# Kernel optimization log

Measured on AMD Instinct MI355X. Metric: run time of the kernel, lower is better.

Reference implementation:

```python
import jax, jax.numpy as jnp
import numpy as np

# Graph sizes: users -> items ('ui') and users -> tags ('ut'), plus reverse etypes.
N_U, N_I, N_T, D = 100000, 50000, 20000, 128
E_UI, E_UT = 500000, 300000


def setup_inputs() -> dict:
    key = jax.random.key(0)
    k = jax.random.split(key, 7)
    return {
        "h_u": jax.random.normal(k[0], (N_U, D), jnp.float32),
        "h_i": jax.random.normal(k[1], (N_I, D), jnp.float32),
        "h_t": jax.random.normal(k[2], (N_T, D), jnp.float32),
        "ui_src": jax.random.randint(k[3], (E_UI,), 0, N_U, jnp.int32),
        "ui_dst": jax.random.randint(k[4], (E_UI,), 0, N_I, jnp.int32),
        "ut_src": jax.random.randint(k[5], (E_UT,), 0, N_U, jnp.int32),
        "ut_dst": jax.random.randint(k[6], (E_UT,), 0, N_T, jnp.int32),
    }


def _seg_sum(x, idx, n):
    return jax.ops.segment_sum(x, idx, num_segments=n)


def _deg(idx, n):
    # in-degree, clamped to min 1 (as torch .clamp(min=1))
    return jnp.clip(_seg_sum(jnp.ones(idx.shape, jnp.float32), idx, n), 1.0, None)


def reference(h_u, h_i, h_t, ui_src, ui_dst, ut_src, ut_dst):
    NORM_2 = -1.0  # default norm_2 arg
    # forward pass: copy_u('h') + sum per etype, then 1/in_degree normalization on dst
    rst_i = _seg_sum(h_u[ui_src], ui_dst, N_I) / _deg(ui_dst, N_I)[:, None]  # [N_I, D]
    rst_t = _seg_sum(h_u[ut_src], ut_dst, N_T) / _deg(ut_dst, N_T)[:, None]  # [N_T, D]
    # backward pass: multi_update_all over reverse etypes, 'sum' cross-etype reducer
    bsrc = _seg_sum(rst_i[ui_dst], ui_src, N_U) + _seg_sum(rst_t[ut_dst], ut_src, N_U)
    # in_degrees_b: per-etype clamped degrees summed across reverse etypes
    deg_b = _deg(ui_src, N_U) + _deg(ut_src, N_U)
    bsrc = bsrc * (deg_b ** NORM_2)[:, None]
    # rst is the LAST etype's normalized dst result ('ut' -> tags)
    return bsrc, rst_t
```

## Files before the change

### kernel.cpp

```cpp
#include <hip/hip_runtime.h>

#define NU 100000
#define NI 50000
#define NT 20000
#define DD 128
#define EUI 500000
#define EUT 300000

#define B_I   0
#define B_T   (NI)
#define B_UUI (NI + NT)
#define B_UUT (NI + NT + NU)
#define NSCAN (NI + NT + NU + NU)
#define TOTAL_E (2 * (EUI + EUT))

#define BPB   512
#define NB    ((NSCAN + BPB - 1) / BPB)
#define CH    8192
#define NBLK  ((TOTAL_E + CH - 1) / CH)
#define NHIST (NB * NBLK)

__device__ __forceinline__ unsigned bfpack(float a, float b) {
    unsigned ua = __float_as_uint(a), ub = __float_as_uint(b);
    ua = (ua + 0x7FFFu + ((ua >> 16) & 1u)) >> 16;
    ub = (ub + 0x7FFFu + ((ub >> 16) & 1u)) >> 16;
    return ua | (ub << 16);
}
__device__ __forceinline__ void bacc(unsigned p, float& a, float& b) {
    a += __uint_as_float(p << 16);
    b += __uint_as_float(p & 0xFFFF0000u);
}

__device__ __forceinline__ void entry_of(int e,
        const int* __restrict__ ui_src, const int* __restrict__ ui_dst,
        const int* __restrict__ ut_src, const int* __restrict__ ut_dst,
        int& bucket, int& val) {
    if (e < EUI)              { bucket = B_I   + ui_dst[e];              val = ui_src[e]; }
    else if (e < 2 * EUI)     { int j = e - EUI;       bucket = B_UUI + ui_src[j]; val = ui_dst[j]; }
    else if (e < 2 * EUI + EUT){ int j = e - 2 * EUI;   bucket = B_T   + ut_dst[j]; val = ut_src[j]; }
    else                      { int j = e - 2 * EUI - EUT; bucket = B_UUT + ut_src[j]; val = ut_dst[j]; }
}

__global__ void k_hist(const int* __restrict__ ui_src, const int* __restrict__ ui_dst,
                       const int* __restrict__ ut_src, const int* __restrict__ ut_dst,
                       int* __restrict__ hist) {
    __shared__ int h[NB];
    int b = blockIdx.x, t = threadIdx.x;
    for (int i = t; i < NB; i += 256) h[i] = 0;
    __syncthreads();
    int e0 = b * CH;
    int e1 = min(e0 + CH, TOTAL_E);
    for (int e = e0 + t; e < e1; e += 256) {
        int bucket, val;
        entry_of(e, ui_src, ui_dst, ut_src, ut_dst, bucket, val);
        (void)val;
        atomicAdd(&h[bucket >> 9], 1);
    }
    __syncthreads();
    for (int i = t; i < NB; i += 256) hist[i * NBLK + b] = h[i];
}

__global__ void k_scanA(int* __restrict__ data, int* __restrict__ bsums, int n) {
    __shared__ int lds[256];
    int b = blockIdx.x, t = threadIdx.x;
    int base = b * 1024 + t * 4;
    int v0 = (base + 0 < n) ? data[base + 0] : 0;
    int v1 = (base + 1 < n) ? data[base + 1] : 0;
    int v2 = (base + 2 < n) ? data[base + 2] : 0;
    int v3 = (base + 3 < n) ? data[base + 3] : 0;
    int i0 = v0, i1 = i0 + v1, i2 = i1 + v2, i3 = i2 + v3;
    lds[t] = i3;
    __syncthreads();
    for (int o = 1; o < 256; o <<= 1) {
        int x = (t >= o) ? lds[t - o] : 0;
        __syncthreads();
        lds[t] += x;
        __syncthreads();
    }
    int ex = lds[t] - i3;
    if (base + 0 < n) data[base + 0] = ex + i0;
    if (base + 1 < n) data[base + 1] = ex + i1;
    if (base + 2 < n) data[base + 2] = ex + i2;
    if (base + 3 < n) data[base + 3] = ex + i3;
    if (t == 255) bsums[b] = lds[255];
}

__global__ void k_scanB(int* __restrict__ bsums, int nsb) {
    __shared__ int lds[512];
    int t = threadIdx.x;
    int a = (t < nsb) ? bsums[t] : 0;
    int b2 = (t + 256 < nsb) ? bsums[t + 256] : 0;
    lds[t] = a;
    lds[t + 256] = b2;
    __syncthreads();
    for (int o = 1; o < 512; o <<= 1) {
        int x0 = (t >= o) ? lds[t - o] : 0;
        int x1 = (t + 256 >= o) ? lds[t + 256 - o] : 0;
        __syncthreads();
        lds[t] += x0;
        lds[t + 256] += x1;
        __syncthreads();
    }
    if (t < nsb) bsums[t] = lds[t] - a;
    if (t + 256 < nsb) bsums[t + 256] = lds[t + 256] - b2;
}

__global__ void k_scanC(int* __restrict__ data, const int* __restrict__ bsums, int n) {
    int b = blockIdx.x;
    int add = bsums[b];
    int base = b * 1024 + threadIdx.x * 4;
    if (base + 0 < n) data[base + 0] += add;
    if (base + 1 < n) data[base + 1] += add;
    if (base + 2 < n) data[base + 2] += add;
    if (base + 3 < n) data[base + 3] += add;
}

__global__ void k_scatterbin(const int* __restrict__ ui_src, const int* __restrict__ ui_dst,
                             const int* __restrict__ ut_src, const int* __restrict__ ut_dst,
                             const int* __restrict__ hist, unsigned* __restrict__ binned) {
    __shared__ int loff[NB];
    int b = blockIdx.x, t = threadIdx.x;
    for (int i = t; i < NB; i += 256) loff[i] = hist[i * NBLK + b];
    __syncthreads();
    int e0 = b * CH;
    int e1 = min(e0 + CH, TOTAL_E);
    for (int e = e0 + t; e < e1; e += 256) {
        int bucket, val;
        entry_of(e, ui_src, ui_dst, ut_src, ut_dst, bucket, val);
        int bin = bucket >> 9;
        int pos = atomicAdd(&loff[bin], -1) - 1;
        binned[pos] = ((unsigned)(bucket & (BPB - 1)) << 17) | (unsigned)val;
    }
}

__global__ void k_bincount(const unsigned* __restrict__ binned,
                           const int* __restrict__ hist, int* __restrict__ off) {
    __shared__ int cnt[BPB];
    int b = blockIdx.x, t = threadIdx.x;
    cnt[t] = 0; cnt[t + 256] = 0;
    __syncthreads();
    int s = (b == 0) ? 0 : hist[b * NBLK - 1];
    int e = hist[(b + 1) * NBLK - 1];
    for (int i = s + t; i < e; i += 256) atomicAdd(&cnt[binned[i] >> 17], 1);
    __syncthreads();
    int base = b * BPB;
    if (base + t < NSCAN) off[base + t] = cnt[t];
    if (base + t + 256 < NSCAN) off[base + t + 256] = cnt[t + 256];
}

__global__ void k_finescatter(const unsigned* __restrict__ binned,
                              const int* __restrict__ hist,
                              int* __restrict__ off, int* __restrict__ edges) {
    __shared__ int loff[BPB];
    int b = blockIdx.x, t = threadIdx.x;
    int base = b * BPB;
    if (base + t < NSCAN) loff[t] = off[base + t];
    if (base + t + 256 < NSCAN) loff[t + 256] = off[base + t + 256];
    __syncthreads();
    int s = (b == 0) ? 0 : hist[b * NBLK - 1];
    int e = hist[(b + 1) * NBLK - 1];
    for (int i = s + t; i < e; i += 256) {
        unsigned v = binned[i];
        int local = v >> 17;
        int pos = atomicAdd(&loff[local], -1) - 1;
        edges[pos] = (int)(v & 0x1FFFFu);
    }
    __syncthreads();
    if (base + t < NSCAN) off[base + t] = loff[t];
    if (base + t + 256 < NSCAN) off[base + t + 256] = loff[t + 256];
}

__global__ void k_cvt(const float4* __restrict__ in, uint4* __restrict__ out) {
    int t = blockIdx.x * blockDim.x + threadIdx.x;
    if (t >= NU * DD / 8) return;
    float4 a = in[t * 2 + 0];
    float4 b = in[t * 2 + 1];
    uint4 o;
    o.x = bfpack(a.x, a.y); o.y = bfpack(a.z, a.w);
    o.z = bfpack(b.x, b.y); o.w = bfpack(b.z, b.w);
    out[t] = o;
}


__global__ void g_fwd(const uint4* __restrict__ feat,
                      const int* __restrict__ off, const int* __restrict__ edges,
                      uint4* __restrict__ rsti_b, uint4* __restrict__ rstt_b,
                      float4* __restrict__ outf) {
    int tid = blockIdx.x * blockDim.x + threadIdx.x;
    int r = tid >> 4;
    int c = tid & 15;
    if (r >= NI + NT) return;
    int start = off[r];
    int end = off[r + 1];
    float a0=0.f,a1=0.f,a2=0.f,a3=0.f,a4=0.f,a5=0.f,a6=0.f,a7=0.f;
    for (int base = start; base < end; base += 16) {
        int n = min(16, end - base);
        int eidx = (c < n) ? edges[base + c] : 0;
        #pragma unroll 4
        for (int k = 0; k < n; ++k) {
            int s = __shfl(eidx, k, 16);
            uint4 p = feat[(size_t)s * 16 + c];
            bacc(p.x, a0, a1); bacc(p.y, a2, a3);
            bacc(p.z, a4, a5); bacc(p.w, a6, a7);
        }
    }
    float inv = 1.0f / fmaxf((float)(end - start), 1.0f);
    a0*=inv; a1*=inv; a2*=inv; a3*=inv; a4*=inv; a5*=inv; a6*=inv; a7*=inv;
    uint4 ob;
    ob.x = bfpack(a0,a1); ob.y = bfpack(a2,a3);
    ob.z = bfpack(a4,a5); ob.w = bfpack(a6,a7);
    if (r < NI) {
        rsti_b[(size_t)r * 16 + c] = ob;
    } else {
        int rt = r - NI;
        rstt_b[(size_t)rt * 16 + c] = ob;
        float4 f0; f0.x=a0; f0.y=a1; f0.z=a2; f0.w=a3;
        float4 f1; f1.x=a4; f1.y=a5; f1.z=a6; f1.w=a7;
        outf[(size_t)rt * 32 + c*2 + 0] = f0;
        outf[(size_t)rt * 32 + c*2 + 1] = f1;
    }
}

__global__ void g_bwd(const uint4* __restrict__ rst_i, const uint4* __restrict__ rst_t,
                      const int* __restrict__ off, const int* __restrict__ edges,
                      float4* __restrict__ bsrc) {
    int tid = blockIdx.x * blockDim.x + threadIdx.x;
    int r = tid >> 4;
    int c = tid & 15;
    if (r >= NU) return;
    int s1 = off[B_UUI + r], e1 = off[B_UUI + r + 1];
    int g2 = B_UUT + r;
    int s2 = off[g2], e2 = (g2 + 1 < NSCAN) ? off[g2 + 1] : TOTAL_E;
    float a0=0.f,a1=0.f,a2=0.f,a3=0.f,a4=0.f,a5=0.f,a6=0.f,a7=0.f;
    for (int base = s1; base < e1; base += 16) {
        int n = min(16, e1 - base);
        int eidx = (c < n) ? edges[base + c] : 0;
        #pragma unroll 4
        for (int k = 0; k < n; ++k) {
            int d = __shfl(eidx, k, 16);
            uint4 p = rst_i[(size_t)d * 16 + c];
            bacc(p.x, a0, a1); bacc(p.y, a2, a3);
            bacc(p.z, a4, a5); bacc(p.w, a6, a7);
        }
    }
    for (int base = s2; base < e2; base += 16) {
        int n = min(16, e2 - base);
        int eidx = (c < n) ? edges[base + c] : 0;
        #pragma unroll 4
        for (int k = 0; k < n; ++k) {
            int d = __shfl(eidx, k, 16);
            uint4 p = rst_t[(size_t)d * 16 + c];
            bacc(p.x, a0, a1); bacc(p.y, a2, a3);
            bacc(p.z, a4, a5); bacc(p.w, a6, a7);
        }
    }
    float inv = 1.0f / (fmaxf((float)(e1 - s1), 1.0f) + fmaxf((float)(e2 - s2), 1.0f));
    float4 f0; f0.x=a0*inv; f0.y=a1*inv; f0.z=a2*inv; f0.w=a3*inv;
    float4 f1; f1.x=a4*inv; f1.y=a5*inv; f1.z=a6*inv; f1.w=a7*inv;
    bsrc[(size_t)r * 32 + c*2 + 0] = f0;
    bsrc[(size_t)r * 32 + c*2 + 1] = f1;
}

__global__ void k_count_old(const int4* __restrict__ ui_src, const int4* __restrict__ ui_dst,
                            const int4* __restrict__ ut_src, const int4* __restrict__ ut_dst,
                            int* __restrict__ off) {
    int i = blockIdx.x * blockDim.x + threadIdx.x;
    if (i < EUI / 4) {
        int4 s = ui_src[i], d = ui_dst[i];
        atomicAdd(&off[B_I + d.x], 1); atomicAdd(&off[B_I + d.y], 1);
        atomicAdd(&off[B_I + d.z], 1); atomicAdd(&off[B_I + d.w], 1);
        atomicAdd(&off[B_UUI + s.x], 1); atomicAdd(&off[B_UUI + s.y], 1);
        atomicAdd(&off[B_UUI + s.z], 1); atomicAdd(&off[B_UUI + s.w], 1);
    } else if (i < EUI / 4 + EUT / 4) {
        int j = i - EUI / 4;
        int4 s = ut_src[j], d = ut_dst[j];
        atomicAdd(&off[B_T + d.x], 1); atomicAdd(&off[B_T + d.y], 1);
        atomicAdd(&off[B_T + d.z], 1); atomicAdd(&off[B_T + d.w], 1);
        atomicAdd(&off[B_UUT + s.x], 1); atomicAdd(&off[B_UUT + s.y], 1);
        atomicAdd(&off[B_UUT + s.z], 1); atomicAdd(&off[B_UUT + s.w], 1);
    }
}

__global__ void k_fill_old(const int2* __restrict__ ui_src, const int2* __restrict__ ui_dst,
                           const int2* __restrict__ ut_src, const int2* __restrict__ ut_dst,
                           int* __restrict__ off, int* __restrict__ edges) {
    int i = blockIdx.x * blockDim.x + threadIdx.x;
    if (i < EUI / 2) {
        int2 s = ui_src[i], d = ui_dst[i];
        edges[atomicAdd(&off[B_I + d.x], -1) - 1] = s.x;
        edges[atomicAdd(&off[B_UUI + s.x], -1) - 1] = d.x;
        edges[atomicAdd(&off[B_I + d.y], -1) - 1] = s.y;
        edges[atomicAdd(&off[B_UUI + s.y], -1) - 1] = d.y;
    } else if (i < EUI / 2 + EUT / 2) {
        int j = i - EUI / 2;
        int2 s = ut_src[j], d = ut_dst[j];
        edges[atomicAdd(&off[B_T + d.x], -1) - 1] = s.x;
        edges[atomicAdd(&off[B_UUT + s.x], -1) - 1] = d.x;
        edges[atomicAdd(&off[B_T + d.y], -1) - 1] = s.y;
        edges[atomicAdd(&off[B_UUT + s.y], -1) - 1] = d.y;
    }
}

__global__ void k_gather_fwd_f(const float4* __restrict__ feat,
                               const int* __restrict__ off, const int* __restrict__ edges,
                               uint2* __restrict__ outb, float4* __restrict__ outf,
                               int base, int nrows) {
    int tid = blockIdx.x * blockDim.x + threadIdx.x;
    int r = tid >> 5;
    int c = tid & 31;
    if (r >= nrows) return;
    int g = base + r;
    int start = off[g];
    int end = (g + 1 < NSCAN) ? off[g + 1] : TOTAL_E;
    float a0 = 0.f, a1 = 0.f, a2 = 0.f, a3 = 0.f;
    for (int e = start; e < end; ++e) {
        float4 v = feat[(size_t)edges[e] * 32 + c];
        a0 += v.x; a1 += v.y; a2 += v.z; a3 += v.w;
    }
    float inv = 1.0f / fmaxf((float)(end - start), 1.0f);
    a0 *= inv; a1 *= inv; a2 *= inv; a3 *= inv;
    uint2 ob; ob.x = bfpack(a0, a1); ob.y = bfpack(a2, a3);
    outb[(size_t)r * 32 + c] = ob;
    if (outf) {
        float4 of; of.x = a0; of.y = a1; of.z = a2; of.w = a3;
        outf[(size_t)r * 32 + c] = of;
    }
}

__global__ void k_gather_bwd_b(const uint2* __restrict__ rst_i,
                               const uint2* __restrict__ rst_t,
                               const int* __restrict__ off, const int* __restrict__ edges,
                               float4* __restrict__ bsrc) {
    int tid = blockIdx.x * blockDim.x + threadIdx.x;
    int r = tid >> 5;
    int c = tid & 31;
    if (r >= NU) return;
    int g1 = B_UUI + r;
    int s1 = off[g1], e1 = off[g1 + 1];
    int g2 = B_UUT + r;
    int s2 = off[g2], e2 = (g2 + 1 < NSCAN) ? off[g2 + 1] : TOTAL_E;
    float a0 = 0.f, a1 = 0.f, a2 = 0.f, a3 = 0.f;
    for (int e = s1; e < e1; ++e) {
        uint2 p = rst_i[(size_t)edges[e] * 32 + c];
        bacc(p.x, a0, a1); bacc(p.y, a2, a3);
    }
    for (int e = s2; e < e2; ++e) {
        uint2 p = rst_t[(size_t)edges[e] * 32 + c];
        bacc(p.x, a0, a1); bacc(p.y, a2, a3);
    }
    float inv = 1.0f / (fmaxf((float)(e1 - s1), 1.0f) + fmaxf((float)(e2 - s2), 1.0f));
    float4 o;
    o.x = a0 * inv; o.y = a1 * inv; o.z = a2 * inv; o.w = a3 * inv;
    bsrc[(size_t)r * 32 + c] = o;
}

__global__ void f_count(const int* __restrict__ ui_src, const int* __restrict__ ui_dst,
                        const int* __restrict__ ut_src, const int* __restrict__ ut_dst,
                        float* __restrict__ cnt_uui, float* __restrict__ cnt_i,
                        float* __restrict__ cnt_uut, float* __restrict__ cnt_t) {
    int i = blockIdx.x * blockDim.x + threadIdx.x;
    if (i < EUI) {
        unsafeAtomicAdd(&cnt_uui[ui_src[i]], 1.0f);
        unsafeAtomicAdd(&cnt_i[ui_dst[i]], 1.0f);
    } else if (i < EUI + EUT) {
        int j = i - EUI;
        unsafeAtomicAdd(&cnt_uut[ut_src[j]], 1.0f);
        unsafeAtomicAdd(&cnt_t[ut_dst[j]], 1.0f);
    }
}
__global__ void f_scatter_fwd(const float4* __restrict__ feat, const int* __restrict__ src,
                              const int* __restrict__ dst, float* __restrict__ out_sum, int nedge) {
    int tid = blockIdx.x * blockDim.x + threadIdx.x;
    int e = tid >> 5, c = tid & 31;
    if (e >= nedge) return;
    float4 v = feat[(size_t)src[e] * 32 + c];
    float* o = out_sum + (size_t)dst[e] * DD + c * 4;
    unsafeAtomicAdd(o + 0, v.x); unsafeAtomicAdd(o + 1, v.y);
    unsafeAtomicAdd(o + 2, v.z); unsafeAtomicAdd(o + 3, v.w);
}
__global__ void f_scatter_bwd(const float4* __restrict__ rst_sum, const float* __restrict__ cnt,
                              const int* __restrict__ src, const int* __restrict__ dst,
                              float* __restrict__ bsrc, int nedge) {
    int tid = blockIdx.x * blockDim.x + threadIdx.x;
    int e = tid >> 5, c = tid & 31;
    if (e >= nedge) return;
    float inv = 1.0f / fmaxf(cnt[dst[e]], 1.0f);
    float4 v = rst_sum[(size_t)dst[e] * 32 + c];
    float* o = bsrc + (size_t)src[e] * DD + c * 4;
    unsafeAtomicAdd(o + 0, v.x * inv); unsafeAtomicAdd(o + 1, v.y * inv);
    unsafeAtomicAdd(o + 2, v.z * inv); unsafeAtomicAdd(o + 3, v.w * inv);
}
__global__ void f_norm(float4* __restrict__ rst, const float* __restrict__ cnt, int nrows) {
    int tid = blockIdx.x * blockDim.x + threadIdx.x;
    int r = tid >> 5, c = tid & 31;
    if (r >= nrows) return;
    float inv = 1.0f / fmaxf(cnt[r], 1.0f);
    float4 v = rst[(size_t)r * 32 + c];
    v.x *= inv; v.y *= inv; v.z *= inv; v.w *= inv;
    rst[(size_t)r * 32 + c] = v;
}
__global__ void f_final(float4* __restrict__ bsrc, const float* __restrict__ cnt_a,
                        const float* __restrict__ cnt_b, int nrows) {
    int tid = blockIdx.x * blockDim.x + threadIdx.x;
    int r = tid >> 5, c = tid & 31;
    if (r >= nrows) return;
    float inv = 1.0f / (fmaxf(cnt_a[r], 1.0f) + fmaxf(cnt_b[r], 1.0f));
    float4 v = bsrc[(size_t)r * 32 + c];
    v.x *= inv; v.y *= inv; v.z *= inv; v.w *= inv;
    bsrc[(size_t)r * 32 + c] = v;
}


extern "C" void kernel_launch(void* const* d_in, const int* in_sizes, int n_in,
                              void* d_out, int out_size, void* d_ws, size_t ws_size,
                              hipStream_t stream) {
    const float* h_u  = (const float*)d_in[0];
    const int* ui_src = (const int*)d_in[3];
    const int* ui_dst = (const int*)d_in[4];
    const int* ut_src = (const int*)d_in[5];
    const int* ut_dst = (const int*)d_in[6];

    float* bsrc  = (float*)d_out;
    float* rst_t = (float*)d_out + (size_t)NU * DD;

    const int B = 256;

    const size_t INT_WORDS = (size_t)NSCAN + 512 + TOTAL_E;
    const size_t BASE_B    = INT_WORDS * 4;
    const size_t HUB_B     = (size_t)NU * DD * 2;
    const size_t RIB_B     = (size_t)NI * DD * 2;
    const size_t RTB_B     = (size_t)NT * DD * 2;
    const size_t NEED_FULL = BASE_B + HUB_B + RIB_B + RTB_B;
    const size_t NEED_HALF = BASE_B + RIB_B + RTB_B;

    if (ws_size >= NEED_FULL) {
        int* off      = (int*)d_ws;
        int* bsums    = off + NSCAN;
        int* edges    = bsums + 512;
        uint4* hu_b   = (uint4*)((char*)d_ws + BASE_B);
        uint4* rsti_b = (uint4*)((char*)d_ws + BASE_B + HUB_B);
        uint4* rstt_b = (uint4*)((char*)d_ws + BASE_B + HUB_B + RIB_B);
        unsigned* binned = (unsigned*)rsti_b;
        int* hist        = (int*)rstt_b;

        k_cvt<<<(NU * DD / 8 + B - 1) / B, B, 0, stream>>>(
            (const float4*)h_u, hu_b);

        k_hist<<<NBLK, B, 0, stream>>>(ui_src, ui_dst, ut_src, ut_dst, hist);

        {
            int nblk = (NHIST + 1023) / 1024;
            k_scanA<<<nblk, B, 0, stream>>>(hist, bsums, NHIST);
            k_scanB<<<1, B, 0, stream>>>(bsums, nblk);
            k_scanC<<<nblk, B, 0, stream>>>(hist, bsums, NHIST);
        }

        k_scatterbin<<<NBLK, B, 0, stream>>>(ui_src, ui_dst, ut_src, ut_dst, hist, binned);

        k_bincount<<<NB, B, 0, stream>>>(binned, hist, off);

        {
            int nblk = (NSCAN + 1023) / 1024;
            k_scanA<<<nblk, B, 0, stream>>>(off, bsums, NSCAN);
            k_scanB<<<1, B, 0, stream>>>(bsums, nblk);
            k_scanC<<<nblk, B, 0, stream>>>(off, bsums, NSCAN);
        }

        k_finescatter<<<NB, B, 0, stream>>>(binned, hist, off, edges);

        g_fwd<<<((long)(NI + NT) * 16 + B - 1) / B, B, 0, stream>>>(
            hu_b, off, edges, rsti_b, rstt_b, (float4*)rst_t);
        g_bwd<<<((long)NU * 16 + B - 1) / B, B, 0, stream>>>(
            rsti_b, rstt_b, off, edges, (float4*)bsrc);
    } else if (ws_size >= NEED_HALF) {
        int* off   = (int*)d_ws;
        int* bsums = off + NSCAN;
        int* edges = bsums + 512;
        uint2* rsti_b = (uint2*)((char*)d_ws + BASE_B);
        uint2* rstt_b = (uint2*)((char*)d_ws + BASE_B + RIB_B);

        hipMemsetAsync(off, 0, (NSCAN + 512) * sizeof(int), stream);

        int nq = EUI / 4 + EUT / 4;
        k_count_old<<<(nq + B - 1) / B, B, 0, stream>>>(
            (const int4*)ui_src, (const int4*)ui_dst,
            (const int4*)ut_src, (const int4*)ut_dst, off);
        {
            int nblk = (NSCAN + 1023) / 1024;
            k_scanA<<<nblk, B, 0, stream>>>(off, bsums, NSCAN);
            k_scanB<<<1, B, 0, stream>>>(bsums, nblk);
            k_scanC<<<nblk, B, 0, stream>>>(off, bsums, NSCAN);
        }
        int nh = EUI / 2 + EUT / 2;
        k_fill_old<<<(nh + B - 1) / B, B, 0, stream>>>(
            (const int2*)ui_src, (const int2*)ui_dst,
            (const int2*)ut_src, (const int2*)ut_dst, off, edges);

        k_gather_fwd_f<<<((long)NI * 32 + B - 1) / B, B, 0, stream>>>(
            (const float4*)h_u, off, edges, rsti_b, (float4*)nullptr, B_I, NI);
        k_gather_fwd_f<<<((long)NT * 32 + B - 1) / B, B, 0, stream>>>(
            (const float4*)h_u, off, edges, rstt_b, (float4*)rst_t, B_T, NT);
        k_gather_bwd_b<<<((long)NU * 32 + B - 1) / B, B, 0, stream>>>(
            rsti_b, rstt_b, off, edges, (float4*)bsrc);
    } else {
        float* ws        = (float*)d_ws;
        float* rst_i_sum = ws;
        float* cnt_i     = rst_i_sum + (size_t)NI * DD;
        float* cnt_t     = cnt_i + NI;
        float* cnt_uui   = cnt_t + NT;
        float* cnt_uut   = cnt_uui + NU;
        size_t ws_floats = (size_t)NI * DD + NI + NT + NU + NU;

        hipMemsetAsync(d_ws, 0, ws_floats * sizeof(float), stream);
        hipMemsetAsync(d_out, 0, (size_t)out_size * sizeof(float), stream);

        int n = EUI + EUT;
        f_count<<<(n + B - 1) / B, B, 0, stream>>>(ui_src, ui_dst, ut_src, ut_dst,
                                                   cnt_uui, cnt_i, cnt_uut, cnt_t);
        f_scatter_fwd<<<((long)EUI * 32 + B - 1) / B, B, 0, stream>>>(
            (const float4*)h_u, ui_src, ui_dst, rst_i_sum, EUI);
        f_scatter_fwd<<<((long)EUT * 32 + B - 1) / B, B, 0, stream>>>(
            (const float4*)h_u, ut_src, ut_dst, rst_t, EUT);
        f_scatter_bwd<<<((long)EUI * 32 + B - 1) / B, B, 0, stream>>>(
            (const float4*)rst_i_sum, cnt_i, ui_src, ui_dst, bsrc, EUI);
        f_scatter_bwd<<<((long)EUT * 32 + B - 1) / B, B, 0, stream>>>(
            (const float4*)rst_t, cnt_t, ut_src, ut_dst, bsrc, EUT);
        f_norm<<<((long)NT * 32 + B - 1) / B, B, 0, stream>>>((float4*)rst_t, cnt_t, NT);
        f_final<<<((long)NU * 32 + B - 1) / B, B, 0, stream>>>((float4*)bsrc, cnt_uui, cnt_uut, NU);
    }
}
```

Measured before the change: 182.7 us.

## Simplify CSR build to global-bin atomics and unroll gather loops by eight

```diff
diff --git a/kernel.cpp b/kernel.cpp
--- a/kernel.cpp
+++ b/kernel.cpp
@@ -18,7 +18,7 @@
 #define NB    ((NSCAN + BPB - 1) / BPB)
 #define CH    8192
 #define NBLK  ((TOTAL_E + CH - 1) / CH)
-#define NHIST (NB * NBLK)
+#define NT3   176
 
 __device__ __forceinline__ unsigned bfpack(float a, float b) {
     unsigned ua = __float_as_uint(a), ub = __float_as_uint(b);
@@ -31,143 +31,124 @@
     b += __uint_as_float(p & 0xFFFF0000u);
 }
 
+__device__ __forceinline__ int bucket_of(int e,
+        const int* __restrict__ ui_src, const int* __restrict__ ui_dst,
+        const int* __restrict__ ut_src, const int* __restrict__ ut_dst) {
+    if (e < EUI)               return B_I   + ui_dst[e];
+    if (e < 2 * EUI)           return B_UUI + ui_src[e - EUI];
+    if (e < 2 * EUI + EUT)     return B_T   + ut_dst[e - 2 * EUI];
+    return B_UUT + ut_src[e - 2 * EUI - EUT];
+}
+
 __device__ __forceinline__ void entry_of(int e,
         const int* __restrict__ ui_src, const int* __restrict__ ui_dst,
         const int* __restrict__ ut_src, const int* __restrict__ ut_dst,
         int& bucket, int& val) {
-    if (e < EUI)              { bucket = B_I   + ui_dst[e];              val = ui_src[e]; }
-    else if (e < 2 * EUI)     { int j = e - EUI;       bucket = B_UUI + ui_src[j]; val = ui_dst[j]; }
-    else if (e < 2 * EUI + EUT){ int j = e - 2 * EUI;   bucket = B_T   + ut_dst[j]; val = ut_src[j]; }
-    else                      { int j = e - 2 * EUI - EUT; bucket = B_UUT + ut_src[j]; val = ut_dst[j]; }
-}
-
-__global__ void k_hist(const int* __restrict__ ui_src, const int* __restrict__ ui_dst,
-                       const int* __restrict__ ut_src, const int* __restrict__ ut_dst,
-                       int* __restrict__ hist) {
+    if (e < EUI)               { bucket = B_I   + ui_dst[e];               val = ui_src[e]; }
+    else if (e < 2 * EUI)      { int j = e - EUI;           bucket = B_UUI + ui_src[j]; val = ui_dst[j]; }
+    else if (e < 2 * EUI + EUT){ int j = e - 2 * EUI;       bucket = B_T   + ut_dst[j]; val = ut_src[j]; }
+    else                       { int j = e - 2 * EUI - EUT; bucket = B_UUT + ut_src[j]; val = ut_dst[j]; }
+}
+
+__global__ void k_hist2(const int* __restrict__ ui_src, const int* __restrict__ ui_dst,
+                        const int* __restrict__ ut_src, const int* __restrict__ ut_dst,
+                        int* __restrict__ gbin) {
     __shared__ int h[NB];
     int b = blockIdx.x, t = threadIdx.x;
     for (int i = t; i < NB; i += 256) h[i] = 0;
     __syncthreads();
     int e0 = b * CH;
     int e1 = min(e0 + CH, TOTAL_E);
+    for (int e = e0 + t; e < e1; e += 256)
+        atomicAdd(&h[bucket_of(e, ui_src, ui_dst, ut_src, ut_dst) >> 9], 1);
+    __syncthreads();
+    for (int i = t; i < NB; i += 256)
+        if (h[i]) atomicAdd(&gbin[i], h[i]);
+}
+
+__global__ void k_scan528(const int* __restrict__ gbin,
+                          int* __restrict__ gstart, int* __restrict__ cursor) {
+    __shared__ int tsum[256];
+    int t = threadIdx.x;
+    int i = t * 3;
+    int v0 = 0, v1 = 0, v2 = 0;
+    if (t < NT3) { v0 = gbin[i]; v1 = gbin[i + 1]; v2 = gbin[i + 2]; }
+    int s = v0 + v1 + v2;
+    tsum[t] = s;
+    __syncthreads();
+    for (int o = 1; o < 256; o <<= 1) {
+        int x = (t >= o) ? tsum[t - o] : 0;
+        __syncthreads();
+        tsum[t] += x;
+        __syncthreads();
+    }
+    int base = tsum[t] - s;
+    if (t < NT3) {
+        gstart[i] = base;                cursor[i] = base;
+        gstart[i + 1] = base + v0;       cursor[i + 1] = base + v0;
+        gstart[i + 2] = base + v0 + v1;  cursor[i + 2] = base + v0 + v1;
+    }
+    if (t == 255) gstart[NB] = tsum[255];
+}
+
+__global__ void k_scatterbin2(const int* __restrict__ ui_src, const int* __restrict__ ui_dst,
+                              const int* __restrict__ ut_src, const int* __restrict__ ut_dst,
+                              int* __restrict__ cursor, unsigned* __restrict__ binned) {
+    __shared__ int h[NB];
+    int b = blockIdx.x, t = threadIdx.x;
+    for (int i = t; i < NB; i += 256) h[i] = 0;
+    __syncthreads();
+    int e0 = b * CH;
+    int e1 = min(e0 + CH, TOTAL_E);
+    for (int e = e0 + t; e < e1; e += 256)
+        atomicAdd(&h[bucket_of(e, ui_src, ui_dst, ut_src, ut_dst) >> 9], 1);
+    __syncthreads();
+    for (int i = t; i < NB; i += 256) {
+        int c = h[i];
+        if (c) h[i] = atomicAdd(&cursor[i], c);
+    }
+    __syncthreads();
     for (int e = e0 + t; e < e1; e += 256) {
         int bucket, val;
         entry_of(e, ui_src, ui_dst, ut_src, ut_dst, bucket, val);
-        (void)val;
-        atomicAdd(&h[bucket >> 9], 1);
-    }
-    __syncthreads();
-    for (int i = t; i < NB; i += 256) hist[i * NBLK + b] = h[i];
-}
-
-__global__ void k_scanA(int* __restrict__ data, int* __restrict__ bsums, int n) {
-    __shared__ int lds[256];
-    int b = blockIdx.x, t = threadIdx.x;
-    int base = b * 1024 + t * 4;
-    int v0 = (base + 0 < n) ? data[base + 0] : 0;
-    int v1 = (base + 1 < n) ? data[base + 1] : 0;
-    int v2 = (base + 2 < n) ? data[base + 2] : 0;
-    int v3 = (base + 3 < n) ? data[base + 3] : 0;
-    int i0 = v0, i1 = i0 + v1, i2 = i1 + v2, i3 = i2 + v3;
-    lds[t] = i3;
-    __syncthreads();
-    for (int o = 1; o < 256; o <<= 1) {
-        int x = (t >= o) ? lds[t - o] : 0;
-        __syncthreads();
-        lds[t] += x;
-        __syncthreads();
-    }
-    int ex = lds[t] - i3;
-    if (base + 0 < n) data[base + 0] = ex + i0;
-    if (base + 1 < n) data[base + 1] = ex + i1;
-    if (base + 2 < n) data[base + 2] = ex + i2;
-    if (base + 3 < n) data[base + 3] = ex + i3;
-    if (t == 255) bsums[b] = lds[255];
-}
-
-__global__ void k_scanB(int* __restrict__ bsums, int nsb) {
-    __shared__ int lds[512];
-    int t = threadIdx.x;
-    int a = (t < nsb) ? bsums[t] : 0;
-    int b2 = (t + 256 < nsb) ? bsums[t + 256] : 0;
-    lds[t] = a;
-    lds[t + 256] = b2;
-    __syncthreads();
-    for (int o = 1; o < 512; o <<= 1) {
-        int x0 = (t >= o) ? lds[t - o] : 0;
-        int x1 = (t + 256 >= o) ? lds[t + 256 - o] : 0;
-        __syncthreads();
-        lds[t] += x0;
-        lds[t + 256] += x1;
-        __syncthreads();
-    }
-    if (t < nsb) bsums[t] = lds[t] - a;
-    if (t + 256 < nsb) bsums[t + 256] = lds[t + 256] - b2;
-}
-
-__global__ void k_scanC(int* __restrict__ data, const int* __restrict__ bsums, int n) {
-    int b = blockIdx.x;
-    int add = bsums[b];
-    int base = b * 1024 + threadIdx.x * 4;
-    if (base + 0 < n) data[base + 0] += add;
-    if (base + 1 < n) data[base + 1] += add;
-    if (base + 2 < n) data[base + 2] += add;
-    if (base + 3 < n) data[base + 3] += add;
-}
-
-__global__ void k_scatterbin(const int* __restrict__ ui_src, const int* __restrict__ ui_dst,
-                             const int* __restrict__ ut_src, const int* __restrict__ ut_dst,
-                             const int* __restrict__ hist, unsigned* __restrict__ binned) {
-    __shared__ int loff[NB];
-    int b = blockIdx.x, t = threadIdx.x;
-    for (int i = t; i < NB; i += 256) loff[i] = hist[i * NBLK + b];
-    __syncthreads();
-    int e0 = b * CH;
-    int e1 = min(e0 + CH, TOTAL_E);
-    for (int e = e0 + t; e < e1; e += 256) {
-        int bucket, val;
-        entry_of(e, ui_src, ui_dst, ut_src, ut_dst, bucket, val);
-        int bin = bucket >> 9;
-        int pos = atomicAdd(&loff[bin], -1) - 1;
+        int pos = atomicAdd(&h[bucket >> 9], 1);
         binned[pos] = ((unsigned)(bucket & (BPB - 1)) << 17) | (unsigned)val;
     }
 }
 
-__global__ void k_bincount(const unsigned* __restrict__ binned,
-                           const int* __restrict__ hist, int* __restrict__ off) {
+__global__ void k_fine(const unsigned* __restrict__ binned, const int* __restrict__ gstart,
+                       int* __restrict__ off, int* __restrict__ edges) {
     __shared__ int cnt[BPB];
+    __shared__ int tsum[256];
     int b = blockIdx.x, t = threadIdx.x;
     cnt[t] = 0; cnt[t + 256] = 0;
     __syncthreads();
-    int s = (b == 0) ? 0 : hist[b * NBLK - 1];
-    int e = hist[(b + 1) * NBLK - 1];
+    int s = gstart[b], e = gstart[b + 1];
     for (int i = s + t; i < e; i += 256) atomicAdd(&cnt[binned[i] >> 17], 1);
     __syncthreads();
-    int base = b * BPB;
-    if (base + t < NSCAN) off[base + t] = cnt[t];
-    if (base + t + 256 < NSCAN) off[base + t + 256] = cnt[t + 256];
-}
-
-__global__ void k_finescatter(const unsigned* __restrict__ binned,
-                              const int* __restrict__ hist,
-                              int* __restrict__ off, int* __restrict__ edges) {
-    __shared__ int loff[BPB];
-    int b = blockIdx.x, t = threadIdx.x;
-    int base = b * BPB;
-    if (base + t < NSCAN) loff[t] = off[base + t];
-    if (base + t + 256 < NSCAN) loff[t + 256] = off[base + t + 256];
-    __syncthreads();
-    int s = (b == 0) ? 0 : hist[b * NBLK - 1];
-    int e = hist[(b + 1) * NBLK - 1];
+    int v0 = cnt[2 * t], v1 = cnt[2 * t + 1];
+    int ps = v0 + v1;
+    tsum[t] = ps;
+    __syncthreads();
+    for (int o = 1; o < 256; o <<= 1) {
+        int x = (t >= o) ? tsum[t - o] : 0;
+        __syncthreads();
+        tsum[t] += x;
+        __syncthreads();
+    }
+    int base = s + tsum[t] - ps;
+    int g0 = b * BPB + 2 * t;
+    if (g0 < NSCAN) off[g0] = base;
+    if (g0 + 1 < NSCAN) off[g0 + 1] = base + v0;
+    __syncthreads();
+    cnt[2 * t] = base;
+    cnt[2 * t + 1] = base + v0;
+    __syncthreads();
     for (int i = s + t; i < e; i += 256) {
         unsigned v = binned[i];
-        int local = v >> 17;
-        int pos = atomicAdd(&loff[local], -1) - 1;
+        int pos = atomicAdd(&cnt[v >> 17], 1);
         edges[pos] = (int)(v & 0x1FFFFu);
     }
-    __syncthreads();
-    if (base + t < NSCAN) off[base + t] = loff[t];
-    if (base + t + 256 < NSCAN) off[base + t + 256] = loff[t + 256];
 }
 
 __global__ void k_cvt(const float4* __restrict__ in, uint4* __restrict__ out) {
@@ -181,6 +162,46 @@
     out[t] = o;
 }
 
+__device__ __forceinline__ void gacc16(const uint4* __restrict__ feat,
+                                       const int* __restrict__ edges,
+                                       int start, int end, int c,
+                                       float& a0, float& a1, float& a2, float& a3,
+                                       float& a4, float& a5, float& a6, float& a7) {
+    for (int base = start; base < end; base += 16) {
+        int n = end - base; if (n > 16) n = 16;
+        int eidx = (c < n) ? edges[base + c] : 0;
+        int k = 0;
+        for (; k + 8 <= n; k += 8) {
+            int s0 = __shfl(eidx, k + 0, 16), s1 = __shfl(eidx, k + 1, 16);
+            int s2 = __shfl(eidx, k + 2, 16), s3 = __shfl(eidx, k + 3, 16);
+            int s4 = __shfl(eidx, k + 4, 16), s5 = __shfl(eidx, k + 5, 16);
+            int s6 = __shfl(eidx, k + 6, 16), s7 = __shfl(eidx, k + 7, 16);
+            uint4 p0 = feat[(size_t)s0 * 16 + c], p1 = feat[(size_t)s1 * 16 + c];
+            uint4 p2 = feat[(size_t)s2 * 16 + c], p3 = feat[(size_t)s3 * 16 + c];
+            uint4 p4 = feat[(size_t)s4 * 16 + c], p5 = feat[(size_t)s5 * 16 + c];
+            uint4 p6 = feat[(size_t)s6 * 16 + c], p7 = feat[(size_t)s7 * 16 + c];
+            bacc(p0.x, a0, a1); bacc(p0.y, a2, a3); bacc(p0.z, a4, a5); bacc(p0.w, a6, a7);
+            bacc(p1.x, a0, a1); bacc(p1.y, a2, a3); bacc(p1.z, a4, a5); bacc(p1.w, a6, a7);
+            bacc(p2.x, a0, a1); bacc(p2.y, a2, a3); bacc(p2.z, a4, a5); bacc(p2.w, a6, a7);
+            bacc(p3.x, a0, a1); bacc(p3.y, a2, a3); bacc(p3.z, a4, a5); bacc(p3.w, a6, a7);
+            bacc(p4.x, a0, a1); bacc(p4.y, a2, a3); bacc(p4.z, a4, a5); bacc(p4.w, a6, a7);
+            bacc(p5.x, a0, a1); bacc(p5.y, a2, a3); bacc(p5.z, a4, a5); bacc(p5.w, a6, a7);
+            bacc(p6.x, a0, a1); bacc(p6.y, a2, a3); bacc(p6.z, a4, a5); bacc(p6.w, a6, a7);
+            bacc(p7.x, a0, a1); bacc(p7.y, a2, a3); bacc(p7.z, a4, a5); bacc(p7.w, a6, a7);
+        }
+        for (; k + 2 <= n; k += 2) {
+            int s0 = __shfl(eidx, k + 0, 16), s1 = __shfl(eidx, k + 1, 16);
+            uint4 p0 = feat[(size_t)s0 * 16 + c], p1 = feat[(size_t)s1 * 16 + c];
+            bacc(p0.x, a0, a1); bacc(p0.y, a2, a3); bacc(p0.z, a4, a5); bacc(p0.w, a6, a7);
+            bacc(p1.x, a0, a1); bacc(p1.y, a2, a3); bacc(p1.z, a4, a5); bacc(p1.w, a6, a7);
+        }
+        if (k < n) {
+            int s0 = __shfl(eidx, k, 16);
+            uint4 p0 = feat[(size_t)s0 * 16 + c];
+            bacc(p0.x, a0, a1); bacc(p0.y, a2, a3); bacc(p0.z, a4, a5); bacc(p0.w, a6, a7);
+        }
+    }
+}
 
 __global__ void g_fwd(const uint4* __restrict__ feat,
                       const int* __restrict__ off, const int* __restrict__ edges,
@@ -193,17 +214,7 @@
     int start = off[r];
     int end = off[r + 1];
     float a0=0.f,a1=0.f,a2=0.f,a3=0.f,a4=0.f,a5=0.f,a6=0.f,a7=0.f;
-    for (int base = start; base < end; base += 16) {
-        int n = min(16, end - base);
-        int eidx = (c < n) ? edges[base + c] : 0;
-        #pragma unroll 4
-        for (int k = 0; k < n; ++k) {
-            int s = __shfl(eidx, k, 16);
-            uint4 p = feat[(size_t)s * 16 + c];
-            bacc(p.x, a0, a1); bacc(p.y, a2, a3);
-            bacc(p.z, a4, a5); bacc(p.w, a6, a7);
-        }
-    }
+    gacc16(feat, edges, start, end, c, a0, a1, a2, a3, a4, a5, a6, a7);
     float inv = 1.0f / fmaxf((float)(end - start), 1.0f);
     a0*=inv; a1*=inv; a2*=inv; a3*=inv; a4*=inv; a5*=inv; a6*=inv; a7*=inv;
     uint4 ob;
@@ -232,33 +243,68 @@
     int g2 = B_UUT + r;
     int s2 = off[g2], e2 = (g2 + 1 < NSCAN) ? off[g2 + 1] : TOTAL_E;
     float a0=0.f,a1=0.f,a2=0.f,a3=0.f,a4=0.f,a5=0.f,a6=0.f,a7=0.f;
-    for (int base = s1; base < e1; base += 16) {
-        int n = min(16, e1 - base);
-        int eidx = (c < n) ? edges[base + c] : 0;
-        #pragma unroll 4
-        for (int k = 0; k < n; ++k) {
-            int d = __shfl(eidx, k, 16);
-            uint4 p = rst_i[(size_t)d * 16 + c];
-            bacc(p.x, a0, a1); bacc(p.y, a2, a3);
-            bacc(p.z, a4, a5); bacc(p.w, a6, a7);
-        }
-    }
-    for (int base = s2; base < e2; base += 16) {
-        int n = min(16, e2 - base);
-        int eidx = (c < n) ? edges[base + c] : 0;
-        #pragma unroll 4
-        for (int k = 0; k < n; ++k) {
-            int d = __shfl(eidx, k, 16);
-            uint4 p = rst_t[(size_t)d * 16 + c];
-            bacc(p.x, a0, a1); bacc(p.y, a2, a3);
-            bacc(p.z, a4, a5); bacc(p.w, a6, a7);
-        }
-    }
+    gacc16(rst_i, edges, s1, e1, c, a0, a1, a2, a3, a4, a5, a6, a7);
+    gacc16(rst_t, edges, s2, e2, c, a0, a1, a2, a3, a4, a5, a6, a7);
     float inv = 1.0f / (fmaxf((float)(e1 - s1), 1.0f) + fmaxf((float)(e2 - s2), 1.0f));
     float4 f0; f0.x=a0*inv; f0.y=a1*inv; f0.z=a2*inv; f0.w=a3*inv;
     float4 f1; f1.x=a4*inv; f1.y=a5*inv; f1.z=a6*inv; f1.w=a7*inv;
     bsrc[(size_t)r * 32 + c*2 + 0] = f0;
     bsrc[(size_t)r * 32 + c*2 + 1] = f1;
+}
+
+__global__ void k_scanA(int* __restrict__ data, int* __restrict__ bsums, int n) {
+    __shared__ int lds[256];
+    int b = blockIdx.x, t = threadIdx.x;
+    int base = b * 1024 + t * 4;
+    int v0 = (base + 0 < n) ? data[base + 0] : 0;
+    int v1 = (base + 1 < n) ? data[base + 1] : 0;
+    int v2 = (base + 2 < n) ? data[base + 2] : 0;
+    int v3 = (base + 3 < n) ? data[base + 3] : 0;
+    int i0 = v0, i1 = i0 + v1, i2 = i1 + v2, i3 = i2 + v3;
+    lds[t] = i3;
+    __syncthreads();
+    for (int o = 1; o < 256; o <<= 1) {
+        int x = (t >= o) ? lds[t - o] : 0;
+        __syncthreads();
+        lds[t] += x;
+        __syncthreads();
+    }
+    int ex = lds[t] - i3;
+    if (base + 0 < n) data[base + 0] = ex + i0;
+    if (base + 1 < n) data[base + 1] = ex + i1;
+    if (base + 2 < n) data[base + 2] = ex + i2;
+    if (base + 3 < n) data[base + 3] = ex + i3;
+    if (t == 255) bsums[b] = lds[255];
+}
+
+__global__ void k_scanB(int* __restrict__ bsums, int nsb) {
+    __shared__ int lds[512];
+    int t = threadIdx.x;
+    int a = (t < nsb) ? bsums[t] : 0;
+    int b2 = (t + 256 < nsb) ? bsums[t + 256] : 0;
+    lds[t] = a;
+    lds[t + 256] = b2;
+    __syncthreads();
+    for (int o = 1; o < 512; o <<= 1) {
+        int x0 = (t >= o) ? lds[t - o] : 0;
+        int x1 = (t + 256 >= o) ? lds[t + 256 - o] : 0;
+        __syncthreads();
+        lds[t] += x0;
+        lds[t + 256] += x1;
+        __syncthreads();
+    }
+    if (t < nsb) bsums[t] = lds[t] - a;
+    if (t + 256 < nsb) bsums[t + 256] = lds[t + 256] - b2;
+}
+
+__global__ void k_scanC(int* __restrict__ data, const int* __restrict__ bsums, int n) {
+    int b = blockIdx.x;
+    int add = bsums[b];
+    int base = b * 1024 + threadIdx.x * 4;
+    if (base + 0 < n) data[base + 0] += add;
+    if (base + 1 < n) data[base + 1] += add;
+    if (base + 2 < n) data[base + 2] += add;
+    if (base + 3 < n) data[base + 3] += add;
 }
 
 __global__ void k_count_old(const int4* __restrict__ ui_src, const int4* __restrict__ ui_dst,
@@ -435,38 +481,26 @@
 
     if (ws_size >= NEED_FULL) {
         int* off      = (int*)d_ws;
-        int* bsums    = off + NSCAN;
+        int* bsums    = off + NSCAN;   (void)bsums;
         int* edges    = bsums + 512;
         uint4* hu_b   = (uint4*)((char*)d_ws + BASE_B);
         uint4* rsti_b = (uint4*)((char*)d_ws + BASE_B + HUB_B);
         uint4* rstt_b = (uint4*)((char*)d_ws + BASE_B + HUB_B + RIB_B);
         unsigned* binned = (unsigned*)rsti_b;
-        int* hist        = (int*)rstt_b;
-
-        k_cvt<<<(NU * DD / 8 + B - 1) / B, B, 0, stream>>>(
-            (const float4*)h_u, hu_b);
-
-        k_hist<<<NBLK, B, 0, stream>>>(ui_src, ui_dst, ut_src, ut_dst, hist);
-
-        {
-            int nblk = (NHIST + 1023) / 1024;
-            k_scanA<<<nblk, B, 0, stream>>>(hist, bsums, NHIST);
-            k_scanB<<<1, B, 0, stream>>>(bsums, nblk);
-            k_scanC<<<nblk, B, 0, stream>>>(hist, bsums, NHIST);
-        }
-
-        k_scatterbin<<<NBLK, B, 0, stream>>>(ui_src, ui_dst, ut_src, ut_dst, hist, binned);
-
-        k_bincount<<<NB, B, 0, stream>>>(binned, hist, off);
-
-        {
-            int nblk = (NSCAN + 1023) / 1024;
-            k_scanA<<<nblk, B, 0, stream>>>(off, bsums, NSCAN);
-            k_scanB<<<1, B, 0, stream>>>(bsums, nblk);
-            k_scanC<<<nblk, B, 0, stream>>>(off, bsums, NSCAN);
-        }
-
-        k_finescatter<<<NB, B, 0, stream>>>(binned, hist, off, edges);
+        int* gbin   = (int*)rstt_b;
+        int* gstart = gbin + NB;
+        int* cursor = gstart + NB + 1;
+
+        k_cvt<<<(NU * DD / 8 + B - 1) / B, B, 0, stream>>>((const float4*)h_u, hu_b);
+
+        hipMemsetAsync(gbin, 0, NB * sizeof(int), stream);
+        k_hist2<<<NBLK, B, 0, stream>>>(ui_src, ui_dst, ut_src, ut_dst, gbin);
+
+        k_scan528<<<1, B, 0, stream>>>(gbin, gstart, cursor);
+
+        k_scatterbin2<<<NBLK, B, 0, stream>>>(ui_src, ui_dst, ut_src, ut_dst, cursor, binned);
+
+        k_fine<<<NB, B, 0, stream>>>(binned, gstart, off, edges);
 
         g_fwd<<<((long)(NI + NT) * 16 + B - 1) / B, B, 0, stream>>>(
             hu_b, off, edges, rsti_b, rstt_b, (float4*)rst_t);
```

Result: faster. 170.7 us (-6.5%).
